# Optimization experiments

Measured on AMD Instinct MI355X. Metric: run time of the kernel, lower is better.

The kernel has to match this reference:

```python
import jax, jax.numpy as jnp
import numpy as np

B, S, T, H, E, K = 32, 256, 256, 4096, 64, 4
GAMMA_ROUTING = 0.5   # gamma_routing init kwarg
TEMPERATURE = 1.0     # routing temperature
EPS = 1e-6


def setup_inputs() -> dict:
    key = jax.random.key(0)
    k1, k2, k3, k4, k5 = jax.random.split(key, 5)
    input_embeds = jax.random.normal(k1, (B, S, H), dtype=jnp.float32)
    prompt_base = 0.02 * jax.random.normal(k2, (T, H), dtype=jnp.float32)
    # module inits delta to zeros; use small noise so routing blend is non-trivial
    prompt_delta = 0.01 * jax.random.normal(k3, (T, H), dtype=jnp.float32)
    LiMEs = 1.0 + jax.random.uniform(k4, (E, H), dtype=jnp.float32, minval=-0.1, maxval=0.1)
    LiME_shared = 0.1 * jax.random.normal(k5, (H,), dtype=jnp.float32)
    gamma = jnp.zeros((1,), dtype=jnp.float32)
    W_proj = jnp.eye(H, dtype=jnp.float32)  # nn.init.eye_ on input_proj.weight
    return {"input_embeds": input_embeds, "prompt_base": prompt_base,
            "prompt_delta": prompt_delta, "LiMEs": LiMEs,
            "LiME_shared": LiME_shared, "gamma": gamma, "W_proj": W_proj}


def reference(input_embeds, prompt_base, prompt_delta, LiMEs, LiME_shared, gamma, W_proj):
    # --- input conditioning (mode='mean' with projection) ---
    cond = jnp.einsum('bsh,oh->bo', input_embeds, W_proj) / input_embeds.shape[1]  # (B,H)
    hidden = prompt_base[None, :, :] + cond[:, None, :]                            # (B,T,H)
    # --- fused routing softmax over first E channels ---
    H_slice = hidden[..., :E]                        # (B,T,E)
    d_slice = prompt_delta[None, :, :E]              # (1,T,E)
    H_scale = jnp.maximum(jnp.max(jnp.abs(H_slice)), EPS)
    d_scale = jnp.maximum(jnp.max(jnp.abs(d_slice)), EPS)
    logits = ((1.0 - GAMMA_ROUTING) * (H_slice / H_scale)
              + GAMMA_ROUTING * (d_slice / d_scale)) / TEMPERATURE
    probs = jax.nn.softmax(logits, axis=-1)          # (B,T,E)
    # --- sparse top-k routing + gather-combine of LiME vectors ---
    topk_vals, topk_idx = jax.lax.top_k(probs, K)    # (B,T,K)
    topk_vals = topk_vals / jnp.maximum(topk_vals.sum(-1, keepdims=True), 1e-9)
    selected = LiMEs[topk_idx]                       # (B,T,K,H) gather
    p_mix = jnp.einsum('btk,btkh->bth', topk_vals, selected)  # (B,T,H)
    # --- blend with shared LiME and apply multiplicative prompt scale ---
    g = jax.nn.sigmoid(gamma)                        # (1,)
    scale = (1.0 - g) * p_mix + g * LiME_shared      # (B,T,H)
    prompt = (prompt_base + prompt_delta)[None, :, :] * scale
    return prompt
```

## Files before the change

kernel.cpp:

```cpp
#include <hip/hip_runtime.h>

#define BB 32
#define SS 256
#define TT 256
#define HH 4096
#define EE 64

typedef unsigned int u32;

__global__ __launch_bounds__(256) void k1_cond(const float* __restrict__ x,
                                               const float* __restrict__ W,
                                               float* __restrict__ cond) {
    __shared__ float X[1024];
    int id = blockIdx.x;
    int hc = id & 3;
    int sc = (id >> 2) & 7;
    int b  = id >> 5;
    int h0 = threadIdx.x * 4;
    int hb = hc * 1024;
    const float* src = x + ((size_t)b * SS + sc * 32) * HH + hb + h0;
    float4 acc = make_float4(0.f, 0.f, 0.f, 0.f);
    for (int s = 0; s < 32; ++s) {
        float4 v = *(const float4*)(src + (size_t)s * HH);
        acc.x += v.x; acc.y += v.y; acc.z += v.z; acc.w += v.w;
    }
    *(float4*)(X + h0) = acc;
    __syncthreads();
    int wave = threadIdx.x >> 6, lane = threadIdx.x & 63;
    for (int e = wave; e < EE; e += 4) {
        const float* wrow = W + (size_t)e * HH + hb;
        float s = 0.f;
#pragma unroll
        for (int i = 0; i < 4; ++i) {
            int h = i * 256 + lane * 4;
            float4 wv = *(const float4*)(wrow + h);
            s += X[h] * wv.x + X[h + 1] * wv.y + X[h + 2] * wv.z + X[h + 3] * wv.w;
        }
#pragma unroll
        for (int off = 32; off; off >>= 1) s += __shfl_xor(s, off);
        if (lane == 0) atomicAdd(cond + b * EE + e, s * (1.0f / SS));
    }
}

__global__ __launch_bounds__(256) void k3_scales(const float* __restrict__ pb,
                                                 const float* __restrict__ pd,
                                                 const float* __restrict__ cond,
                                                 u32* __restrict__ scaleBits) {
    int tid = blockIdx.x * 256 + threadIdx.x;
    float hmax = 0.f, dmax = 0.f;
    for (int idx = tid; idx < BB * TT * EE; idx += 32768) {
        int e = idx & 63, t = (idx >> 6) & 255, b = idx >> 14;
        float v = pb[t * HH + e] + cond[b * EE + e];
        hmax = fmaxf(hmax, fabsf(v));
    }
    for (int idx = tid; idx < TT * EE; idx += 32768) {
        int e = idx & 63, t = idx >> 6;
        dmax = fmaxf(dmax, fabsf(pd[t * HH + e]));
    }
#pragma unroll
    for (int off = 32; off; off >>= 1) {
        hmax = fmaxf(hmax, __shfl_xor(hmax, off));
        dmax = fmaxf(dmax, __shfl_xor(dmax, off));
    }
    __shared__ float sh[4], sd[4];
    int wave = threadIdx.x >> 6, lane = threadIdx.x & 63;
    if (lane == 0) { sh[wave] = hmax; sd[wave] = dmax; }
    __syncthreads();
    if (threadIdx.x == 0) {
        float h = sh[0], d = sd[0];
#pragma unroll
        for (int i = 1; i < 4; ++i) { h = fmaxf(h, sh[i]); d = fmaxf(d, sd[i]); }
        atomicMax(scaleBits + 0, __float_as_uint(h));
        atomicMax(scaleBits + 1, __float_as_uint(d));
    }
}

__global__ __launch_bounds__(256) void k4_main(const float* __restrict__ pb,
                                               const float* __restrict__ pd,
                                               const float* __restrict__ limes,
                                               const float* __restrict__ shr,
                                               const float* __restrict__ gamma,
                                               const float* __restrict__ cond,
                                               const u32* __restrict__ scaleBits,
                                               float* __restrict__ out) {
    int wave = threadIdx.x >> 6, lane = threadIdx.x & 63;
    int row = blockIdx.x * 4 + wave;
    int b = row >> 8, t = row & 255;

    float Hs = fmaxf(__uint_as_float(scaleBits[0]), 1e-6f);
    float Ds = fmaxf(__uint_as_float(scaleBits[1]), 1e-6f);
    float g = 1.f / (1.f + __expf(-gamma[0]));

    size_t rb = (size_t)t * HH;
    float logit = 0.5f * (pb[rb + lane] + cond[b * EE + lane]) / Hs
                + 0.5f * pd[rb + lane] / Ds;

    int selIdx[4]; float selL[4];
    float work = logit;
#pragma unroll
    for (int k = 0; k < 4; ++k) {
        float v = work; int vi = lane;
#pragma unroll
        for (int off = 32; off; off >>= 1) {
            float ov = __shfl_xor(v, off);
            int   oi = __shfl_xor(vi, off);
            if (ov > v || (ov == v && oi < vi)) { v = ov; vi = oi; }
        }
        selIdx[k] = vi; selL[k] = v;
        if (lane == vi) work = -1e30f;
    }
    float m = selL[0];
    float w0 = __expf(selL[0] - m), w1 = __expf(selL[1] - m);
    float w2 = __expf(selL[2] - m), w3 = __expf(selL[3] - m);
    float inv = 1.f / (w0 + w1 + w2 + w3);
    w0 *= inv; w1 *= inv; w2 *= inv; w3 *= inv;

    const float* L0 = limes + (size_t)selIdx[0] * HH;
    const float* L1 = limes + (size_t)selIdx[1] * HH;
    const float* L2 = limes + (size_t)selIdx[2] * HH;
    const float* L3 = limes + (size_t)selIdx[3] * HH;
    size_t ob = (size_t)row * HH;
    float one_m_g = 1.f - g;

    for (int i = 0; i < 16; ++i) {
        int h = i * 256 + lane * 4;
        float4 fb = *(const float4*)(pb + rb + h);
        float4 fd = *(const float4*)(pd + rb + h);
        float4 f0 = *(const float4*)(L0 + h);
        float4 f1 = *(const float4*)(L1 + h);
        float4 f2 = *(const float4*)(L2 + h);
        float4 f3 = *(const float4*)(L3 + h);
        float4 fs = *(const float4*)(shr + h);
        float4 r;
        float pm;
        pm = w0 * f0.x + w1 * f1.x + w2 * f2.x + w3 * f3.x;
        r.x = (fb.x + fd.x) * (one_m_g * pm + g * fs.x);
        pm = w0 * f0.y + w1 * f1.y + w2 * f2.y + w3 * f3.y;
        r.y = (fb.y + fd.y) * (one_m_g * pm + g * fs.y);
        pm = w0 * f0.z + w1 * f1.z + w2 * f2.z + w3 * f3.z;
        r.z = (fb.z + fd.z) * (one_m_g * pm + g * fs.z);
        pm = w0 * f0.w + w1 * f1.w + w2 * f2.w + w3 * f3.w;
        r.w = (fb.w + fd.w) * (one_m_g * pm + g * fs.w);
        *(float4*)(out + ob + h) = r;
    }
}

extern "C" void kernel_launch(void* const* d_in, const int* in_sizes, int n_in,
                              void* d_out, int out_size, void* d_ws, size_t ws_size,
                              hipStream_t stream) {
    const float *x = 0, *pb = 0, *pd = 0, *limes = 0, *shr = 0, *gm = 0, *W = 0;
    for (int i = 0; i < n_in; ++i) {
        const float* p = (const float*)d_in[i];
        switch (in_sizes[i]) {
            case BB * SS * HH: x = p; break;
            case TT * HH: if (!pb) pb = p; else pd = p; break;
            case EE * HH: limes = p; break;
            case HH: shr = p; break;
            case 1: gm = p; break;
            case HH * HH: W = p; break;
        }
    }
    float* out = (float*)d_out;

    u32* scaleBits = (u32*)d_ws;
    float* cond = (float*)d_ws + 2;

    hipMemsetAsync(d_ws, 0, (2 + BB * EE) * sizeof(float), stream);
    k1_cond<<<BB * 8 * 4, 256, 0, stream>>>(x, W, cond);
    k3_scales<<<128, 256, 0, stream>>>(pb, pd, cond, scaleBits);
    k4_main<<<BB * TT / 4, 256, 0, stream>>>(pb, pd, limes, shr, gm, cond,
                                             scaleBits, out);
}
```

Baseline: 353.4 us.

## Precompute prompt sum and gated shared vector; use nontemporal loads and stores

Adds a prep stage that writes pb+pd and sigmoid(gamma)*shared into workspace, so the main kernel reads one prompt row instead of two and folds the gating into the expert weights. The cond reduction now uses nontemporal streaming loads with unrolling, and the output goes out through nontemporal stores. The main kernel gets launch bounds with a minimum of 4 blocks. This saves per-row loads at the cost of an extra pass over T×H and a workspace size check, with the old path kept as a fallback.

```diff
diff --git a/kernel.cpp b/kernel.cpp
--- a/kernel.cpp
+++ b/kernel.cpp
@@ -7,6 +7,7 @@
 #define EE 64
 
 typedef unsigned int u32;
+typedef float f4 __attribute__((ext_vector_type(4)));
 
 __global__ __launch_bounds__(256) void k1_cond(const float* __restrict__ x,
                                                const float* __restrict__ W,
@@ -19,12 +20,13 @@
     int h0 = threadIdx.x * 4;
     int hb = hc * 1024;
     const float* src = x + ((size_t)b * SS + sc * 32) * HH + hb + h0;
-    float4 acc = make_float4(0.f, 0.f, 0.f, 0.f);
+    f4 acc = 0.f;
+#pragma unroll 8
     for (int s = 0; s < 32; ++s) {
-        float4 v = *(const float4*)(src + (size_t)s * HH);
-        acc.x += v.x; acc.y += v.y; acc.z += v.z; acc.w += v.w;
-    }
-    *(float4*)(X + h0) = acc;
+        f4 v = __builtin_nontemporal_load((const f4*)(src + (size_t)s * HH));
+        acc += v;
+    }
+    *(f4*)(X + h0) = acc;
     __syncthreads();
     int wave = threadIdx.x >> 6, lane = threadIdx.x & 63;
     for (int e = wave; e < EE; e += 4) {
@@ -33,8 +35,10 @@
 #pragma unroll
         for (int i = 0; i < 4; ++i) {
             int h = i * 256 + lane * 4;
-            float4 wv = *(const float4*)(wrow + h);
-            s += X[h] * wv.x + X[h + 1] * wv.y + X[h + 2] * wv.z + X[h + 3] * wv.w;
+            f4 wv = *(const f4*)(wrow + h);
+            f4 xv = *(const f4*)(X + h);
+            f4 p = wv * xv;
+            s += p.x + p.y + p.z + p.w;
         }
 #pragma unroll
         for (int off = 32; off; off >>= 1) s += __shfl_xor(s, off);
@@ -42,11 +46,38 @@
     }
 }
 
-__global__ __launch_bounds__(256) void k3_scales(const float* __restrict__ pb,
-                                                 const float* __restrict__ pd,
-                                                 const float* __restrict__ cond,
-                                                 u32* __restrict__ scaleBits) {
-    int tid = blockIdx.x * 256 + threadIdx.x;
+__global__ __launch_bounds__(256) void k3_prep(const float* __restrict__ pb,
+                                               const float* __restrict__ pd,
+                                               const float* __restrict__ shr,
+                                               const float* __restrict__ gamma,
+                                               const float* __restrict__ cond,
+                                               u32* __restrict__ scaleBits,
+                                               float* __restrict__ pbd,
+                                               float* __restrict__ gshr,
+                                               int fuse) {
+    int bid = blockIdx.x;
+    if (fuse) {
+        if (bid < TT) {
+            size_t rb = (size_t)bid * HH;
+            const f4* a = (const f4*)(pb + rb);
+            const f4* c = (const f4*)(pd + rb);
+            f4* o = (f4*)(pbd + rb);
+#pragma unroll
+            for (int i = 0; i < 4; ++i) {
+                int j = i * 256 + threadIdx.x;
+                o[j] = a[j] + c[j];
+            }
+            return;
+        }
+        if (bid < TT + 4) {
+            int j = (bid - TT) * 256 + threadIdx.x;
+            float g = 1.f / (1.f + __expf(-gamma[0]));
+            ((f4*)gshr)[j] = g * ((const f4*)shr)[j];
+            return;
+        }
+    }
+    int sb = fuse ? (TT + 4) : 0;
+    int tid = (bid - sb) * 256 + threadIdx.x;
     float hmax = 0.f, dmax = 0.f;
     for (int idx = tid; idx < BB * TT * EE; idx += 32768) {
         int e = idx & 63, t = (idx >> 6) & 255, b = idx >> 14;
@@ -75,14 +106,17 @@
     }
 }
 
-__global__ __launch_bounds__(256) void k4_main(const float* __restrict__ pb,
-                                               const float* __restrict__ pd,
-                                               const float* __restrict__ limes,
-                                               const float* __restrict__ shr,
-                                               const float* __restrict__ gamma,
-                                               const float* __restrict__ cond,
-                                               const u32* __restrict__ scaleBits,
-                                               float* __restrict__ out) {
+template<int FUSE>
+__global__ __launch_bounds__(256, 4) void k4_main(const float* __restrict__ pb,
+                                                  const float* __restrict__ pd,
+                                                  const float* __restrict__ limes,
+                                                  const float* __restrict__ shr,
+                                                  const float* __restrict__ gamma,
+                                                  const float* __restrict__ cond,
+                                                  const u32* __restrict__ scaleBits,
+                                                  const float* __restrict__ pbd,
+                                                  const float* __restrict__ gshr,
+                                                  float* __restrict__ out) {
     int wave = threadIdx.x >> 6, lane = threadIdx.x & 63;
     int row = blockIdx.x * 4 + wave;
     int b = row >> 8, t = row & 255;
@@ -120,28 +154,39 @@
     const float* L2 = limes + (size_t)selIdx[2] * HH;
     const float* L3 = limes + (size_t)selIdx[3] * HH;
     size_t ob = (size_t)row * HH;
-    float one_m_g = 1.f - g;
-
-    for (int i = 0; i < 16; ++i) {
-        int h = i * 256 + lane * 4;
-        float4 fb = *(const float4*)(pb + rb + h);
-        float4 fd = *(const float4*)(pd + rb + h);
-        float4 f0 = *(const float4*)(L0 + h);
-        float4 f1 = *(const float4*)(L1 + h);
-        float4 f2 = *(const float4*)(L2 + h);
-        float4 f3 = *(const float4*)(L3 + h);
-        float4 fs = *(const float4*)(shr + h);
-        float4 r;
-        float pm;
-        pm = w0 * f0.x + w1 * f1.x + w2 * f2.x + w3 * f3.x;
-        r.x = (fb.x + fd.x) * (one_m_g * pm + g * fs.x);
-        pm = w0 * f0.y + w1 * f1.y + w2 * f2.y + w3 * f3.y;
-        r.y = (fb.y + fd.y) * (one_m_g * pm + g * fs.y);
-        pm = w0 * f0.z + w1 * f1.z + w2 * f2.z + w3 * f3.z;
-        r.z = (fb.z + fd.z) * (one_m_g * pm + g * fs.z);
-        pm = w0 * f0.w + w1 * f1.w + w2 * f2.w + w3 * f3.w;
-        r.w = (fb.w + fd.w) * (one_m_g * pm + g * fs.w);
-        *(float4*)(out + ob + h) = r;
+    float om = 1.f - g;
+
+    if (FUSE) {
+        float c0 = w0 * om, c1 = w1 * om, c2 = w2 * om, c3 = w3 * om;
+        const float* P = pbd + rb;
+#pragma unroll
+        for (int i = 0; i < 16; ++i) {
+            int h = i * 256 + lane * 4;
+            f4 fp = *(const f4*)(P + h);
+            f4 f0 = *(const f4*)(L0 + h);
+            f4 f1 = *(const f4*)(L1 + h);
+            f4 f2 = *(const f4*)(L2 + h);
+            f4 f3 = *(const f4*)(L3 + h);
+            f4 fg = *(const f4*)(gshr + h);
+            f4 mix = fg + c0 * f0 + c1 * f1 + c2 * f2 + c3 * f3;
+            f4 r = fp * mix;
+            __builtin_nontemporal_store(r, (f4*)(out + ob + h));
+        }
+    } else {
+#pragma unroll
+        for (int i = 0; i < 16; ++i) {
+            int h = i * 256 + lane * 4;
+            f4 fb = *(const f4*)(pb + rb + h);
+            f4 fd = *(const f4*)(pd + rb + h);
+            f4 f0 = *(const f4*)(L0 + h);
+            f4 f1 = *(const f4*)(L1 + h);
+            f4 f2 = *(const f4*)(L2 + h);
+            f4 f3 = *(const f4*)(L3 + h);
+            f4 fs = *(const f4*)(shr + h);
+            f4 pm = w0 * f0 + w1 * f1 + w2 * f2 + w3 * f3;
+            f4 r = (fb + fd) * (om * pm + g * fs);
+            __builtin_nontemporal_store(r, (f4*)(out + ob + h));
+        }
     }
 }
 
@@ -164,10 +209,20 @@
 
     u32* scaleBits = (u32*)d_ws;
     float* cond = (float*)d_ws + 2;
+    float* gshr = (float*)d_ws + 2 + BB * EE;
+    float* pbd  = gshr + HH;
+    size_t need = (size_t)(2 + BB * EE + HH) * sizeof(float)
+                + (size_t)TT * HH * sizeof(float);
+    int fuse = (ws_size >= need) ? 1 : 0;
 
     hipMemsetAsync(d_ws, 0, (2 + BB * EE) * sizeof(float), stream);
     k1_cond<<<BB * 8 * 4, 256, 0, stream>>>(x, W, cond);
-    k3_scales<<<128, 256, 0, stream>>>(pb, pd, cond, scaleBits);
-    k4_main<<<BB * TT / 4, 256, 0, stream>>>(pb, pd, limes, shr, gm, cond,
-                                             scaleBits, out);
-}
+    k3_prep<<<fuse ? (TT + 4 + 128) : 128, 256, 0, stream>>>(pb, pd, shr, gm, cond,
+                                                             scaleBits, pbd, gshr, fuse);
+    if (fuse)
+        k4_main<1><<<BB * TT / 4, 256, 0, stream>>>(pb, pd, limes, shr, gm, cond,
+                                                    scaleBits, pbd, gshr, out);
+    else
+        k4_main<0><<<BB * TT / 4, 256, 0, stream>>>(pb, pd, limes, shr, gm, cond,
+                                                    scaleBits, pbd, gshr, out);
+}
```

Measured after the change: 310.6 us. 12.1% less time.

## Stage per-token prompt and shared gate in LDS, nontemporal streaming loads/stores

Applied to the files above, without the earlier changes.

k4_main now assigns one token t to each block, covering four batch rows per wave group across 8 blocks per token. Each block stages pb+pd and g*shared into LDS once and reuses them across its waves, so the per-row global reloads of pb, pd and shr go away. The gate factor (1-g) is folded into the top-k weights. The output store and the input_embeds loads in k1 are now nontemporal, and both kernels get launch_bounds occupancy hints. The cost is 32KB of LDS per block, which may limit occupancy, and a different block-to-output mapping that changes write locality.

```diff
diff --git a/kernel.cpp b/kernel.cpp
--- a/kernel.cpp
+++ b/kernel.cpp
@@ -7,10 +7,11 @@
 #define EE 64
 
 typedef unsigned int u32;
+typedef float f4 __attribute__((ext_vector_type(4)));
 
-__global__ __launch_bounds__(256) void k1_cond(const float* __restrict__ x,
-                                               const float* __restrict__ W,
-                                               float* __restrict__ cond) {
+__global__ __launch_bounds__(256, 4) void k1_cond(const float* __restrict__ x,
+                                                  const float* __restrict__ W,
+                                                  float* __restrict__ cond) {
     __shared__ float X[1024];
     int id = blockIdx.x;
     int hc = id & 3;
@@ -19,12 +20,13 @@
     int h0 = threadIdx.x * 4;
     int hb = hc * 1024;
     const float* src = x + ((size_t)b * SS + sc * 32) * HH + hb + h0;
-    float4 acc = make_float4(0.f, 0.f, 0.f, 0.f);
+    f4 acc = 0.f;
+#pragma unroll 8
     for (int s = 0; s < 32; ++s) {
-        float4 v = *(const float4*)(src + (size_t)s * HH);
-        acc.x += v.x; acc.y += v.y; acc.z += v.z; acc.w += v.w;
+        f4 v = __builtin_nontemporal_load((const f4*)(src + (size_t)s * HH));
+        acc += v;
     }
-    *(float4*)(X + h0) = acc;
+    *(f4*)(X + h0) = acc;
     __syncthreads();
     int wave = threadIdx.x >> 6, lane = threadIdx.x & 63;
     for (int e = wave; e < EE; e += 4) {
@@ -33,8 +35,10 @@
 #pragma unroll
         for (int i = 0; i < 4; ++i) {
             int h = i * 256 + lane * 4;
-            float4 wv = *(const float4*)(wrow + h);
-            s += X[h] * wv.x + X[h + 1] * wv.y + X[h + 2] * wv.z + X[h + 3] * wv.w;
+            f4 wv = *(const f4*)(wrow + h);
+            f4 xv = *(const f4*)(X + h);
+            f4 p = wv * xv;
+            s += p.x + p.y + p.z + p.w;
         }
 #pragma unroll
         for (int off = 32; off; off >>= 1) s += __shfl_xor(s, off);
@@ -75,23 +79,43 @@
     }
 }
 
-__global__ __launch_bounds__(256) void k4_main(const float* __restrict__ pb,
-                                               const float* __restrict__ pd,
-                                               const float* __restrict__ limes,
-                                               const float* __restrict__ shr,
-                                               const float* __restrict__ gamma,
-                                               const float* __restrict__ cond,
-                                               const u32* __restrict__ scaleBits,
-                                               float* __restrict__ out) {
+__global__ __launch_bounds__(256, 4) void k4_main(const float* __restrict__ pb,
+                                                  const float* __restrict__ pd,
+                                                  const float* __restrict__ limes,
+                                                  const float* __restrict__ shr,
+                                                  const float* __restrict__ gamma,
+                                                  const float* __restrict__ cond,
+                                                  const u32* __restrict__ scaleBits,
+                                                  float* __restrict__ out) {
+    __shared__ float Pbd[HH];
+    __shared__ float Gs[HH];
+    int t  = blockIdx.x >> 3;
+    int bq = blockIdx.x & 7;
+    float g = 1.f / (1.f + __expf(-gamma[0]));
+    size_t rb = (size_t)t * HH;
+
+    {
+        const f4* Pb = (const f4*)(pb + rb);
+        const f4* Pd = (const f4*)(pd + rb);
+        const f4* Sh = (const f4*)shr;
+#pragma unroll
+        for (int i = 0; i < 4; ++i) {
+            int j = i * 256 + threadIdx.x;
+            f4 a = Pb[j];
+            f4 c = Pd[j];
+            f4 s = Sh[j];
+            ((f4*)Pbd)[j] = a + c;
+            ((f4*)Gs)[j]  = g * s;
+        }
+    }
+    __syncthreads();
+
     int wave = threadIdx.x >> 6, lane = threadIdx.x & 63;
-    int row = blockIdx.x * 4 + wave;
-    int b = row >> 8, t = row & 255;
+    int b = bq * 4 + wave;
 
     float Hs = fmaxf(__uint_as_float(scaleBits[0]), 1e-6f);
     float Ds = fmaxf(__uint_as_float(scaleBits[1]), 1e-6f);
-    float g = 1.f / (1.f + __expf(-gamma[0]));
 
-    size_t rb = (size_t)t * HH;
     float logit = 0.5f * (pb[rb + lane] + cond[b * EE + lane]) / Hs
                 + 0.5f * pd[rb + lane] / Ds;
 
@@ -113,35 +137,28 @@
     float w0 = __expf(selL[0] - m), w1 = __expf(selL[1] - m);
     float w2 = __expf(selL[2] - m), w3 = __expf(selL[3] - m);
     float inv = 1.f / (w0 + w1 + w2 + w3);
-    w0 *= inv; w1 *= inv; w2 *= inv; w3 *= inv;
+    float om = 1.f - g;
+    float c0 = w0 * inv * om, c1 = w1 * inv * om;
+    float c2 = w2 * inv * om, c3 = w3 * inv * om;
 
     const float* L0 = limes + (size_t)selIdx[0] * HH;
     const float* L1 = limes + (size_t)selIdx[1] * HH;
     const float* L2 = limes + (size_t)selIdx[2] * HH;
     const float* L3 = limes + (size_t)selIdx[3] * HH;
-    size_t ob = (size_t)row * HH;
-    float one_m_g = 1.f - g;
+    size_t ob = ((size_t)b * TT + t) * HH;
 
+#pragma unroll
     for (int i = 0; i < 16; ++i) {
         int h = i * 256 + lane * 4;
-        float4 fb = *(const float4*)(pb + rb + h);
-        float4 fd = *(const float4*)(pd + rb + h);
-        float4 f0 = *(const float4*)(L0 + h);
-        float4 f1 = *(const float4*)(L1 + h);
-        float4 f2 = *(const float4*)(L2 + h);
-        float4 f3 = *(const float4*)(L3 + h);
-        float4 fs = *(const float4*)(shr + h);
-        float4 r;
-        float pm;
-        pm = w0 * f0.x + w1 * f1.x + w2 * f2.x + w3 * f3.x;
-        r.x = (fb.x + fd.x) * (one_m_g * pm + g * fs.x);
-        pm = w0 * f0.y + w1 * f1.y + w2 * f2.y + w3 * f3.y;
-        r.y = (fb.y + fd.y) * (one_m_g * pm + g * fs.y);
-        pm = w0 * f0.z + w1 * f1.z + w2 * f2.z + w3 * f3.z;
-        r.z = (fb.z + fd.z) * (one_m_g * pm + g * fs.z);
-        pm = w0 * f0.w + w1 * f1.w + w2 * f2.w + w3 * f3.w;
-        r.w = (fb.w + fd.w) * (one_m_g * pm + g * fs.w);
-        *(float4*)(out + ob + h) = r;
+        f4 fp = *(const f4*)(Pbd + h);
+        f4 fg = *(const f4*)(Gs + h);
+        f4 f0 = *(const f4*)(L0 + h);
+        f4 f1 = *(const f4*)(L1 + h);
+        f4 f2 = *(const f4*)(L2 + h);
+        f4 f3 = *(const f4*)(L3 + h);
+        f4 mix = fg + c0 * f0 + c1 * f1 + c2 * f2 + c3 * f3;
+        f4 r = fp * mix;
+        __builtin_nontemporal_store(r, (f4*)(out + ob + h));
     }
 }
 
```

Measured after the change: 310.1 us. -12.2%, faster.
